# Optimization experiments

Measured on AMD Instinct MI355X. Metric: run time of the kernel, lower is better.

The kernel has to match this reference:

```python
import jax, jax.numpy as jnp
import numpy as np

B, C, H, W = 8, 384, 32, 32
NH = 6
HD = C // NH          # 64
T = H * W             # 1024
EPS = 1e-5            # torch InstanceNorm2d default


def setup_inputs() -> dict:
    key = jax.random.key(0)
    ks = jax.random.split(key, 8)
    s = 1.0 / np.sqrt(C)  # keep pre-softmax logits in a sane range
    x = jax.random.normal(ks[0], (B, C, H, W), dtype=jnp.float32)
    Wq = jax.random.normal(ks[1], (C, C), dtype=jnp.float32) * s
    Wk = jax.random.normal(ks[2], (C, C), dtype=jnp.float32) * s
    Wv = jax.random.normal(ks[3], (C, C), dtype=jnp.float32) * s
    head_w = jax.random.normal(ks[4], (NH, NH), dtype=jnp.float32) * (1.0 / np.sqrt(NH))
    gamma = jnp.ones((NH,), dtype=jnp.float32)
    beta = jnp.zeros((NH,), dtype=jnp.float32)
    projW = jax.random.normal(ks[5], (C, C), dtype=jnp.float32) * s
    projb = jnp.zeros((C,), dtype=jnp.float32)
    return {"x": x, "Wq": Wq, "Wk": Wk, "Wv": Wv, "head_w": head_w,
            "gamma": gamma, "beta": beta, "projW": projW, "projb": projb}


def reference(x, Wq, Wk, Wv, head_w, gamma, beta, projW, projb):
    b, c, h, w = x.shape
    t = h * w
    scale = HD ** (-0.5)
    xf = x.reshape(b, c, t)                               # [B,C,T]
    # 1x1 convs == channel GEMMs; conv weight [Cout,Cin]
    q = jnp.einsum('oc,bct->bot', Wq, xf).reshape(b, NH, HD, t)
    k = jnp.einsum('oc,bct->bot', Wk, xf).reshape(b, NH, HD, t)
    v = jnp.einsum('oc,bct->bot', Wv, xf).reshape(b, NH, HD, t)
    # raw scores [B,h,T,T], scaled
    scores = jnp.einsum('bhdq,bhdt->bhqt', q, k) * scale
    # cross-head 1x1 conv mix: out-head g from in-head h
    mixed = jnp.einsum('gh,bhqt->bgqt', head_w, scores)
    attn = jax.nn.softmax(mixed, axis=-1)
    # InstanceNorm2d over spatial dims (q,T) per (b,head), biased variance
    mean = jnp.mean(attn, axis=(2, 3), keepdims=True)
    var = jnp.var(attn, axis=(2, 3), keepdims=True)
    attn = (attn - mean) * jax.lax.rsqrt(var + EPS)
    attn = attn * gamma[None, :, None, None] + beta[None, :, None, None]
    # value matmul: v is [B,h,d,T]
    out = jnp.einsum('bhqt,bhdt->bhqd', attn, v)          # [B,h,T,d]
    # faithful row-major reshape (matches torch .view(B, T, C))
    out = out.reshape(b, t, c)
    y = out @ projW.T + projb                              # Linear(C,C)
    return jnp.transpose(y, (0, 2, 1)).reshape(b, c, h, w)
```

## Files before the change

kernel.cpp:

```cpp
#include <hip/hip_runtime.h>
#include <hip/hip_bf16.h>
#include <cstdint>

typedef __bf16 bf16_t;
typedef __bf16 bf16x8 __attribute__((ext_vector_type(8)));
typedef float  f32x4  __attribute__((ext_vector_type(4)));

#define MFMA16(a, b, c) __builtin_amdgcn_mfma_f32_16x16x32_bf16((a), (b), (c), 0, 0, 0)

constexpr int BB = 8, CC = 384, NHH = 6, TT = 1024;

union U8 { uint4 u; bf16_t h[8]; };
union U2 { unsigned int u; bf16_t h[2]; };

struct CastArgs {
    const void* src[9];
    bf16_t*     dst[9];
    int         n[9];
};

__global__ __launch_bounds__(256) void cast_kernel(CastArgs a)
{
    const bool isbf = (((const unsigned short*)a.src[5])[0] == 0x3F80u);
    const int ai = blockIdx.y;
    const int n  = a.n[ai];
    bf16_t* dst  = a.dst[ai];
    const int t0     = (blockIdx.x * 256 + threadIdx.x) * 8;
    const int stride = gridDim.x * 256 * 8;
    if (isbf) {
        const bf16_t* s = (const bf16_t*)a.src[ai];
        for (int idx = t0; idx < n; idx += stride) {
            if (idx + 8 <= n) *(uint4*)(dst + idx) = *(const uint4*)(s + idx);
            else for (int j = 0; idx + j < n; ++j) dst[idx + j] = s[idx + j];
        }
    } else {
        const float* s = (const float*)a.src[ai];
        for (int idx = t0; idx < n; idx += stride) {
            if (idx + 8 <= n) {
                f32x4 v0 = *(const f32x4*)(s + idx);
                f32x4 v1 = *(const f32x4*)(s + idx + 4);
                U8 o;
                #pragma unroll
                for (int j = 0; j < 4; ++j) { o.h[j] = (bf16_t)v0[j]; o.h[4 + j] = (bf16_t)v1[j]; }
                *(uint4*)(dst + idx) = o.u;
            } else for (int j = 0; idx + j < n; ++j) dst[idx + j] = (bf16_t)s[idx + j];
        }
    }
}

__global__ __launch_bounds__(256) void qkv_kernel(
    const bf16_t* __restrict__ x,
    const bf16_t* __restrict__ Wq,
    const bf16_t* __restrict__ Wk,
    const bf16_t* __restrict__ Wv,
    const bf16_t* __restrict__ head_w,
    bf16_t* __restrict__ Qmix,
    bf16_t* __restrict__ kT,
    bf16_t* __restrict__ vm)
{
    const int og = blockIdx.x;
    const int tt = blockIdx.y;
    const int b  = blockIdx.z;
    const int t0 = tt * 64;
    const int tid  = threadIdx.x;
    const int lane = tid & 63;
    const int wid  = tid >> 6;
    const int quad = lane >> 4;
    const int l16  = lane & 15;

    __shared__ __align__(16) bf16_t xT[64][CC + 8];
    __shared__ float smixL[36];

    if (tid < 36) smixL[tid] = 0.125f * (float)head_w[tid];
    {
        const bf16_t* xb = x + (size_t)b * CC * TT;
        const int tq = tid & 7;
        const int cp = tid >> 3;
        #pragma unroll
        for (int pass = 0; pass < 6; ++pass) {
            const int c = (pass * 32 + cp) * 2;
            U8 r0, r1;
            r0.u = *(const uint4*)(xb + (size_t)c * TT + t0 + tq * 8);
            r1.u = *(const uint4*)(xb + (size_t)(c + 1) * TT + t0 + tq * 8);
            #pragma unroll
            for (int j = 0; j < 8; ++j) {
                U2 p; p.h[0] = r0.h[j]; p.h[1] = r1.h[j];
                *(unsigned int*)&xT[tq * 8 + j][c] = p.u;
            }
        }
    }
    __syncthreads();

    const bf16_t* W = (og < 2) ? Wq : (og < 4) ? Wk : Wv;
    const int obase = (og & 1) * 192 + wid * 48;

    if (og < 4) {
        f32x4 acc[3][4];
        const f32x4 zero = {0.f, 0.f, 0.f, 0.f};
        #pragma unroll
        for (int mi = 0; mi < 3; ++mi)
            #pragma unroll
            for (int ni = 0; ni < 4; ++ni) acc[mi][ni] = zero;

        for (int k0 = 0; k0 < CC; k0 += 32) {
            bf16x8 afr[3];
            #pragma unroll
            for (int mi = 0; mi < 3; ++mi)
                afr[mi] = *(const bf16x8*)(W + (size_t)(obase + mi * 16 + l16) * CC + k0 + quad * 8);
            #pragma unroll
            for (int ni = 0; ni < 4; ++ni) {
                bf16x8 bfr = *(const bf16x8*)&xT[ni * 16 + l16][k0 + quad * 8];
                #pragma unroll
                for (int mi = 0; mi < 3; ++mi)
                    acc[mi][ni] = MFMA16(afr[mi], bfr, acc[mi][ni]);
            }
        }

        if (og < 2) {
            for (int g = 0; g < 6; ++g) {
                bf16_t* dst = Qmix + (size_t)(b * NHH + g) * TT * CC;
                #pragma unroll
                for (int mi = 0; mi < 3; ++mi)
                    #pragma unroll
                    for (int ni = 0; ni < 4; ++ni) {
                        const int o0 = obase + mi * 16 + quad * 4;
                        const int tl = t0 + ni * 16 + l16;
                        const float m = smixL[g * 6 + (o0 >> 6)];
                        U2 lo2, hi2;
                        lo2.h[0] = (bf16_t)(acc[mi][ni][0] * m); lo2.h[1] = (bf16_t)(acc[mi][ni][1] * m);
                        hi2.h[0] = (bf16_t)(acc[mi][ni][2] * m); hi2.h[1] = (bf16_t)(acc[mi][ni][3] * m);
                        uint2 pk; pk.x = lo2.u; pk.y = hi2.u;
                        *(uint2*)(dst + (size_t)tl * CC + o0) = pk;
                    }
            }
        } else {
            #pragma unroll
            for (int mi = 0; mi < 3; ++mi)
                #pragma unroll
                for (int ni = 0; ni < 4; ++ni) {
                    const int o0 = obase + mi * 16 + quad * 4;
                    const int tl = t0 + ni * 16 + l16;
                    U2 lo2, hi2;
                    lo2.h[0] = (bf16_t)acc[mi][ni][0]; lo2.h[1] = (bf16_t)acc[mi][ni][1];
                    hi2.h[0] = (bf16_t)acc[mi][ni][2]; hi2.h[1] = (bf16_t)acc[mi][ni][3];
                    uint2 pk; pk.x = lo2.u; pk.y = hi2.u;
                    *(uint2*)(kT + ((size_t)b * TT + tl) * CC + o0) = pk;
                }
        }
    } else {
        f32x4 acc[4][3];
        const f32x4 zero = {0.f, 0.f, 0.f, 0.f};
        #pragma unroll
        for (int mi = 0; mi < 4; ++mi)
            #pragma unroll
            for (int ni = 0; ni < 3; ++ni) acc[mi][ni] = zero;

        for (int k0 = 0; k0 < CC; k0 += 32) {
            bf16x8 bfr[3];
            #pragma unroll
            for (int ni = 0; ni < 3; ++ni)
                bfr[ni] = *(const bf16x8*)(W + (size_t)(obase + ni * 16 + l16) * CC + k0 + quad * 8);
            #pragma unroll
            for (int mi = 0; mi < 4; ++mi) {
                bf16x8 afr = *(const bf16x8*)&xT[mi * 16 + l16][k0 + quad * 8];
                #pragma unroll
                for (int ni = 0; ni < 3; ++ni)
                    acc[mi][ni] = MFMA16(afr, bfr[ni], acc[mi][ni]);
            }
        }

        #pragma unroll
        for (int mi = 0; mi < 4; ++mi)
            #pragma unroll
            for (int ni = 0; ni < 3; ++ni) {
                const int ol  = obase + ni * 16 + l16;
                const int tl0 = mi * 16 + quad * 4;
                U2 lo2, hi2;
                lo2.h[0] = (bf16_t)acc[mi][ni][0]; lo2.h[1] = (bf16_t)acc[mi][ni][1];
                hi2.h[0] = (bf16_t)acc[mi][ni][2]; hi2.h[1] = (bf16_t)acc[mi][ni][3];
                uint2 pk; pk.x = lo2.u; pk.y = hi2.u;
                *(uint2*)(vm + ((size_t)b * CC + ol) * TT + t0 + tl0) = pk;
            }
    }
}

__global__ __launch_bounds__(256) void vrow_kernel(const bf16_t* __restrict__ vm,
                                                   float* __restrict__ vrs)
{
    const int bg = blockIdx.x;
    const int d  = threadIdx.x & 63;
    const int qr = threadIdx.x >> 6;
    const bf16_t* row = vm + ((size_t)(bg / 6) * CC + (bg % 6) * 64 + d) * TT + qr * 256;
    float s = 0.f;
    for (int i = 0; i < 256; i += 8) {
        U8 v; v.u = *(const uint4*)(row + i);
        #pragma unroll
        for (int j = 0; j < 8; ++j) s += (float)v.h[j];
    }
    __shared__ float red[4][64];
    red[qr][d] = s;
    __syncthreads();
    if (qr == 0) vrs[bg * 64 + d] = red[0][d] + red[1][d] + red[2][d] + red[3][d];
}

__global__ __launch_bounds__(256, 3) void fused_attn(
    const bf16_t* __restrict__ Qmix,
    const bf16_t* __restrict__ kT,
    const bf16_t* __restrict__ vm,
    float* __restrict__ Uhat,
    float* __restrict__ sumsq)
{
    const int L  = blockIdx.x;
    const int b  = L & 7;
    const int rr = L >> 3;
    const int qt = rr & 15;
    const int g  = rr >> 4;
    const int qbase = qt * 64;
    const int tid = threadIdx.x, lane = tid & 63, wid = tid >> 6;
    const int quad = lane >> 4, l16 = lane & 15;
    const int Msub = (wid & 1) * 64;
    const int Nsub = (wid >> 1) * 32;

    __shared__ __align__(16) bf16_t sm[12288];
    bf16_t* At = sm;
    bf16_t* Bt = sm + 8192;
    bf16_t* Ps = sm;
    bf16_t* Vt = sm + 4096;
    __shared__ float lred[4][2][16], l2red[4][2][16];
    __shared__ float lrowS[64];

    const bf16_t* kTb = kT + (size_t)b * TT * CC;
    const bf16_t* Qb  = Qmix + ((size_t)(b * NHH + g) * TT + qbase) * CC;
    const bf16_t* Vb  = vm + ((size_t)b * CC + g * 64) * TT;

    float lacc[2] = {0.f, 0.f}, l2acc[2] = {0.f, 0.f};
    f32x4 U[4];
    const f32x4 zero = {0.f, 0.f, 0.f, 0.f};
    #pragma unroll
    for (int n2 = 0; n2 < 4; ++n2) U[n2] = zero;

    for (int tt = 0; tt < 8; ++tt) {
        f32x4 S[4][2];
        #pragma unroll
        for (int mi = 0; mi < 4; ++mi)
            #pragma unroll
            for (int ni = 0; ni < 2; ++ni) S[mi][ni] = zero;

        for (int kk = 0; kk < 6; ++kk) {
            __syncthreads();
            #pragma unroll
            for (int it = 0; it < 4; ++it) {
                const int id = it * 256 + tid;
                const int row = id >> 3, ch = id & 7;
                U8 v; v.u = *(const uint4*)(kTb + (size_t)(tt * 128 + row) * CC + kk * 64 + ch * 8);
                *(uint4*)&At[row * 64 + ((ch ^ (row & 7)) * 8)] = v.u;
            }
            #pragma unroll
            for (int it = 0; it < 2; ++it) {
                const int id = it * 256 + tid;
                const int row = id >> 3, ch = id & 7;
                U8 v; v.u = *(const uint4*)(Qb + (size_t)row * CC + kk * 64 + ch * 8);
                *(uint4*)&Bt[row * 64 + ((ch ^ (row & 7)) * 8)] = v.u;
            }
            __syncthreads();
            #pragma unroll
            for (int k2 = 0; k2 < 2; ++k2) {
                const int sw = ((k2 * 4 + quad) ^ (l16 & 7)) * 8;
                bf16x8 a[4], bq[2];
                #pragma unroll
                for (int mi = 0; mi < 4; ++mi)
                    a[mi] = *(const bf16x8*)&At[(Msub + mi * 16 + l16) * 64 + sw];
                #pragma unroll
                for (int ni = 0; ni < 2; ++ni)
                    bq[ni] = *(const bf16x8*)&Bt[(Nsub + ni * 16 + l16) * 64 + sw];
                #pragma unroll
                for (int mi = 0; mi < 4; ++mi)
                    #pragma unroll
                    for (int ni = 0; ni < 2; ++ni)
                        S[mi][ni] = MFMA16(a[mi], bq[ni], S[mi][ni]);
            }
        }

        #pragma unroll
        for (int mi = 0; mi < 4; ++mi)
            #pragma unroll
            for (int ni = 0; ni < 2; ++ni)
                #pragma unroll
                for (int r = 0; r < 4; ++r) {
                    const float p = __expf(fminf(S[mi][ni][r], 60.0f));
                    S[mi][ni][r] = p;
                    lacc[ni]  += p;
                    l2acc[ni] += p * p;
                }

        __syncthreads();

        #pragma unroll
        for (int it = 0; it < 4; ++it) {
            const int id = it * 256 + tid;
            const int row = id >> 4, ch = id & 15;
            U8 v; v.u = *(const uint4*)(Vb + (size_t)row * TT + tt * 128 + ch * 8);
            *(uint4*)&Vt[row * 128 + ((((ch & 7) ^ (row & 7)) | (ch & 8)) * 8)] = v.u;
        }

        #pragma unroll
        for (int h = 0; h < 2; ++h) {
            if ((wid & 1) == h) {
                #pragma unroll
                for (int mi = 0; mi < 4; ++mi) {
                    const int tc = mi * 2 + (quad >> 1);
                    #pragma unroll
                    for (int ni = 0; ni < 2; ++ni) {
                        const int q = Nsub + ni * 16 + l16;
                        U2 lo2, hi2;
                        lo2.h[0] = (bf16_t)S[mi][ni][0]; lo2.h[1] = (bf16_t)S[mi][ni][1];
                        hi2.h[0] = (bf16_t)S[mi][ni][2]; hi2.h[1] = (bf16_t)S[mi][ni][3];
                        uint2 pk; pk.x = lo2.u; pk.y = hi2.u;
                        *(uint2*)&Ps[q * 64 + ((tc ^ (l16 & 7)) * 8) + (quad & 1) * 4] = pk;
                    }
                }
            }
            __syncthreads();
            bf16x8 ap[2];
            #pragma unroll
            for (int k2 = 0; k2 < 2; ++k2) {
                const int qa = wid * 16 + l16;
                ap[k2] = *(const bf16x8*)&Ps[qa * 64 + (((k2 * 4 + quad) ^ (l16 & 7)) * 8)];
            }
            #pragma unroll
            for (int n2 = 0; n2 < 4; ++n2) {
                const int d = n2 * 16 + l16;
                #pragma unroll
                for (int k2 = 0; k2 < 2; ++k2) {
                    const int tc = h * 8 + k2 * 4 + quad;
                    bf16x8 bv = *(const bf16x8*)&Vt[d * 128 + ((((tc & 7) ^ (l16 & 7)) | (tc & 8)) * 8)];
                    U[n2] = MFMA16(ap[k2], bv, U[n2]);
                }
            }
            __syncthreads();
        }
    }

    #pragma unroll
    for (int ni = 0; ni < 2; ++ni) {
        float l = lacc[ni], l2 = l2acc[ni];
        l  += __shfl_xor(l, 16, 64);  l  += __shfl_xor(l, 32, 64);
        l2 += __shfl_xor(l2, 16, 64); l2 += __shfl_xor(l2, 32, 64);
        if (quad == 0) { lred[wid][ni][l16] = l; l2red[wid][ni][l16] = l2; }
    }
    __syncthreads();
    if (tid < 64) {
        const int q = tid;
        const int w0 = (q >> 5) * 2, ni = (q >> 4) & 1, lo = q & 15;
        const float l  = lred[w0][ni][lo]  + lred[w0 + 1][ni][lo];
        const float l2 = l2red[w0][ni][lo] + l2red[w0 + 1][ni][lo];
        lrowS[q] = l;
        float c = l2 / (l * l);
        #pragma unroll
        for (int off = 1; off < 64; off <<= 1) c += __shfl_xor(c, off, 64);
        if (tid == 0) atomicAdd(&sumsq[b * NHH + g], c);
    }
    __syncthreads();

    float* Ub = Uhat + ((size_t)(b * NHH + g) * TT + qbase) * 64;
    #pragma unroll
    for (int r = 0; r < 4; ++r) {
        const int ql = wid * 16 + quad * 4 + r;
        const float invl = 1.0f / lrowS[ql];
        #pragma unroll
        for (int n2 = 0; n2 < 4; ++n2)
            Ub[(size_t)ql * 64 + n2 * 16 + l16] = U[n2][r] * invl;
    }
}

__global__ __launch_bounds__(256) void proj_kernel(
    const float* __restrict__ Uhat,
    const float* __restrict__ vrs,
    const float* __restrict__ sumsq,
    const bf16_t* __restrict__ gamma,
    const bf16_t* __restrict__ beta,
    const bf16_t* __restrict__ projW,
    const bf16_t* __restrict__ projb,
    float* __restrict__ out)
{
    const int ts = blockIdx.x;
    const int b  = blockIdx.y;
    const int t0 = ts * 32;
    const int tid = threadIdx.x, lane = tid & 63, wid = tid >> 6;
    const int quad = lane >> 4, l16 = lane & 15;

    __shared__ float Ac[6], Cc[6], pb[CC];
    if (tid < 6) {
        const float ss  = sumsq[b * NHH + tid];
        const float var = fmaxf(ss - 1.0f, 0.0f) * (1.0f / 1048576.0f);
        const float a   = (float)gamma[tid] * rsqrtf(var + 1e-5f);
        Ac[tid] = a;
        Cc[tid] = (float)beta[tid] - a * (1.0f / 1024.0f);
    }
    for (int i = tid; i < CC; i += 256) pb[i] = (float)projb[i];
    __syncthreads();

    f32x4 acc[6][2];
    const f32x4 zero = {0.f, 0.f, 0.f, 0.f};
    #pragma unroll
    for (int mi = 0; mi < 6; ++mi)
        #pragma unroll
        for (int ni = 0; ni < 2; ++ni) acc[mi][ni] = zero;

    const float* Ub = Uhat + (size_t)b * TT * CC;
    for (int k0 = 0; k0 < CC; k0 += 32) {
        bf16x8 bfr[2];
        #pragma unroll
        for (int ni = 0; ni < 2; ++ni) {
            const int tl = t0 + ni * 16 + l16;
            const int baseoff = tl * CC + k0 + quad * 8;
            f32x4 u0 = *(const f32x4*)(Ub + baseoff);
            f32x4 u1 = *(const f32x4*)(Ub + baseoff + 4);
            U8 z;
            #pragma unroll
            for (int j = 0; j < 8; ++j) {
                const int off = baseoff + j;
                const int h = off >> 16;
                const int d = off & 63;
                const float uv = (j < 4) ? u0[j] : u1[j - 4];
                z.h[j] = (bf16_t)(Ac[h] * uv + Cc[h] * vrs[(b * NHH + h) * 64 + d]);
            }
            bfr[ni] = *(const bf16x8*)&z;
        }
        #pragma unroll
        for (int mi = 0; mi < 6; ++mi) {
            const int o = wid * 96 + mi * 16 + l16;
            bf16x8 afr = *(const bf16x8*)(projW + (size_t)o * CC + k0 + quad * 8);
            #pragma unroll
            for (int ni = 0; ni < 2; ++ni)
                acc[mi][ni] = MFMA16(afr, bfr[ni], acc[mi][ni]);
        }
    }

    #pragma unroll
    for (int mi = 0; mi < 6; ++mi)
        #pragma unroll
        for (int ni = 0; ni < 2; ++ni)
            #pragma unroll
            for (int r = 0; r < 4; ++r) {
                const int o  = wid * 96 + mi * 16 + quad * 4 + r;
                const int tl = t0 + ni * 16 + l16;
                out[((size_t)b * CC + o) * TT + tl] = acc[mi][ni][r] + pb[o];
            }
}

extern "C" void kernel_launch(void* const* d_in, const int* in_sizes, int n_in,
                              void* d_out, int out_size, void* d_ws, size_t ws_size,
                              hipStream_t stream)
{
    float* outp = (float*)d_out;
    char* ws = (char*)d_ws;

    size_t off = 0;
    auto alloc = [&](size_t bytes) {
        void* p = ws + off;
        off += (bytes + 255) & ~(size_t)255;
        return p;
    };

    const size_t szQ = (size_t)BB * TT * CC * sizeof(bf16_t);

    bf16_t* cx  = (bf16_t*)alloc(szQ);
    bf16_t* cWq = (bf16_t*)alloc((size_t)CC * CC * 2);
    bf16_t* cWk = (bf16_t*)alloc((size_t)CC * CC * 2);
    bf16_t* cWv = (bf16_t*)alloc((size_t)CC * CC * 2);
    bf16_t* cPW = (bf16_t*)alloc((size_t)CC * CC * 2);
    bf16_t* chw = (bf16_t*)alloc(64 * 2);
    bf16_t* cg  = (bf16_t*)alloc(64 * 2);
    bf16_t* cb  = (bf16_t*)alloc(64 * 2);
    bf16_t* cpb = (bf16_t*)alloc(CC * 2);
    bf16_t* Qm  = (bf16_t*)alloc((size_t)BB * NHH * TT * CC * 2);
    bf16_t* kT  = (bf16_t*)alloc(szQ);
    bf16_t* vm  = (bf16_t*)alloc(szQ);
    float*  Uh  = (float*)alloc((size_t)BB * NHH * TT * 64 * 4);
    float*  vr  = (float*)alloc(48 * 64 * 4);
    float*  sq  = (float*)alloc(48 * 4);

    CastArgs ca;
    bf16_t* dsts[9] = {cx, cWq, cWk, cWv, chw, cg, cb, cPW, cpb};
    for (int i = 0; i < 9; ++i) {
        ca.src[i] = d_in[i];
        ca.dst[i] = dsts[i];
        ca.n[i]   = in_sizes[i];
    }

    hipMemsetAsync(sq, 0, 48 * sizeof(float), stream);
    cast_kernel<<<dim3(192, 9), 256, 0, stream>>>(ca);
    qkv_kernel<<<dim3(6, 16, 8), 256, 0, stream>>>(cx, cWq, cWk, cWv, chw, Qm, kT, vm);
    vrow_kernel<<<48, 256, 0, stream>>>(vm, vr);
    fused_attn<<<768, 256, 0, stream>>>(Qm, kT, vm, Uh, sq);
    proj_kernel<<<dim3(32, 8), 256, 0, stream>>>(Uh, vr, sq, cg, cb, cPW, cpb, outp);
}
```

Baseline: 217.7 us.

## Apply head mix in attention kernel, prefetch tiles, fuse V row sums

The head-mixed Q tensor (six copies per batch) is no longer materialized in the QKV kernel. A single unmixed Q is written, and the attention kernel scales it by the head-mix weights while staging it into shared memory. The attention kernel also prefetches the next K/Q tiles and V tiles into registers so global loads overlap compute. The P·V stage now uses a single 128-wide P tile, which drops two barriers per iteration but enlarges shared memory. The separate vrow kernel is folded into the QKV epilogue through atomics, and the memset now covers vrs plus sumsq, which relies on them being allocated next to each other.

```diff
diff --git a/kernel.cpp b/kernel.cpp
--- a/kernel.cpp
+++ b/kernel.cpp
@@ -53,10 +53,10 @@
     const bf16_t* __restrict__ Wq,
     const bf16_t* __restrict__ Wk,
     const bf16_t* __restrict__ Wv,
-    const bf16_t* __restrict__ head_w,
-    bf16_t* __restrict__ Qmix,
+    bf16_t* __restrict__ qT,
     bf16_t* __restrict__ kT,
-    bf16_t* __restrict__ vm)
+    bf16_t* __restrict__ vm,
+    float* __restrict__ vrs)
 {
     const int og = blockIdx.x;
     const int tt = blockIdx.y;
@@ -69,9 +69,7 @@
     const int l16  = lane & 15;
 
     __shared__ __align__(16) bf16_t xT[64][CC + 8];
-    __shared__ float smixL[36];
-
-    if (tid < 36) smixL[tid] = 0.125f * (float)head_w[tid];
+
     {
         const bf16_t* xb = x + (size_t)b * CC * TT;
         const int tq = tid & 7;
@@ -116,37 +114,19 @@
             }
         }
 
-        if (og < 2) {
-            for (int g = 0; g < 6; ++g) {
-                bf16_t* dst = Qmix + (size_t)(b * NHH + g) * TT * CC;
-                #pragma unroll
-                for (int mi = 0; mi < 3; ++mi)
-                    #pragma unroll
-                    for (int ni = 0; ni < 4; ++ni) {
-                        const int o0 = obase + mi * 16 + quad * 4;
-                        const int tl = t0 + ni * 16 + l16;
-                        const float m = smixL[g * 6 + (o0 >> 6)];
-                        U2 lo2, hi2;
-                        lo2.h[0] = (bf16_t)(acc[mi][ni][0] * m); lo2.h[1] = (bf16_t)(acc[mi][ni][1] * m);
-                        hi2.h[0] = (bf16_t)(acc[mi][ni][2] * m); hi2.h[1] = (bf16_t)(acc[mi][ni][3] * m);
-                        uint2 pk; pk.x = lo2.u; pk.y = hi2.u;
-                        *(uint2*)(dst + (size_t)tl * CC + o0) = pk;
-                    }
-            }
-        } else {
-            #pragma unroll
-            for (int mi = 0; mi < 3; ++mi)
-                #pragma unroll
-                for (int ni = 0; ni < 4; ++ni) {
-                    const int o0 = obase + mi * 16 + quad * 4;
-                    const int tl = t0 + ni * 16 + l16;
-                    U2 lo2, hi2;
-                    lo2.h[0] = (bf16_t)acc[mi][ni][0]; lo2.h[1] = (bf16_t)acc[mi][ni][1];
-                    hi2.h[0] = (bf16_t)acc[mi][ni][2]; hi2.h[1] = (bf16_t)acc[mi][ni][3];
-                    uint2 pk; pk.x = lo2.u; pk.y = hi2.u;
-                    *(uint2*)(kT + ((size_t)b * TT + tl) * CC + o0) = pk;
-                }
-        }
+        bf16_t* dst = (og < 2) ? qT : kT;
+        #pragma unroll
+        for (int mi = 0; mi < 3; ++mi)
+            #pragma unroll
+            for (int ni = 0; ni < 4; ++ni) {
+                const int o0 = obase + mi * 16 + quad * 4;
+                const int tl = t0 + ni * 16 + l16;
+                U2 lo2, hi2;
+                lo2.h[0] = (bf16_t)acc[mi][ni][0]; lo2.h[1] = (bf16_t)acc[mi][ni][1];
+                hi2.h[0] = (bf16_t)acc[mi][ni][2]; hi2.h[1] = (bf16_t)acc[mi][ni][3];
+                uint2 pk; pk.x = lo2.u; pk.y = hi2.u;
+                *(uint2*)(dst + ((size_t)b * TT + tl) * CC + o0) = pk;
+            }
     } else {
         f32x4 acc[4][3];
         const f32x4 zero = {0.f, 0.f, 0.f, 0.f};
@@ -170,43 +150,31 @@
         }
 
         #pragma unroll
-        for (int mi = 0; mi < 4; ++mi)
-            #pragma unroll
-            for (int ni = 0; ni < 3; ++ni) {
-                const int ol  = obase + ni * 16 + l16;
+        for (int ni = 0; ni < 3; ++ni) {
+            const int ol = obase + ni * 16 + l16;
+            float s = 0.f;
+            #pragma unroll
+            for (int mi = 0; mi < 4; ++mi) {
                 const int tl0 = mi * 16 + quad * 4;
                 U2 lo2, hi2;
                 lo2.h[0] = (bf16_t)acc[mi][ni][0]; lo2.h[1] = (bf16_t)acc[mi][ni][1];
                 hi2.h[0] = (bf16_t)acc[mi][ni][2]; hi2.h[1] = (bf16_t)acc[mi][ni][3];
                 uint2 pk; pk.x = lo2.u; pk.y = hi2.u;
                 *(uint2*)(vm + ((size_t)b * CC + ol) * TT + t0 + tl0) = pk;
-            }
+                s += acc[mi][ni][0] + acc[mi][ni][1] + acc[mi][ni][2] + acc[mi][ni][3];
+            }
+            s += __shfl_xor(s, 16, 64);
+            s += __shfl_xor(s, 32, 64);
+            if (quad == 0) atomicAdd(&vrs[b * CC + ol], s);
+        }
     }
 }
 
-__global__ __launch_bounds__(256) void vrow_kernel(const bf16_t* __restrict__ vm,
-                                                   float* __restrict__ vrs)
-{
-    const int bg = blockIdx.x;
-    const int d  = threadIdx.x & 63;
-    const int qr = threadIdx.x >> 6;
-    const bf16_t* row = vm + ((size_t)(bg / 6) * CC + (bg % 6) * 64 + d) * TT + qr * 256;
-    float s = 0.f;
-    for (int i = 0; i < 256; i += 8) {
-        U8 v; v.u = *(const uint4*)(row + i);
-        #pragma unroll
-        for (int j = 0; j < 8; ++j) s += (float)v.h[j];
-    }
-    __shared__ float red[4][64];
-    red[qr][d] = s;
-    __syncthreads();
-    if (qr == 0) vrs[bg * 64 + d] = red[0][d] + red[1][d] + red[2][d] + red[3][d];
-}
-
 __global__ __launch_bounds__(256, 3) void fused_attn(
-    const bf16_t* __restrict__ Qmix,
+    const bf16_t* __restrict__ qT,
     const bf16_t* __restrict__ kT,
     const bf16_t* __restrict__ vm,
+    const bf16_t* __restrict__ head_w,
     float* __restrict__ Uhat,
     float* __restrict__ sumsq)
 {
@@ -221,17 +189,25 @@
     const int Msub = (wid & 1) * 64;
     const int Nsub = (wid >> 1) * 32;
 
-    __shared__ __align__(16) bf16_t sm[12288];
+    __shared__ __align__(16) bf16_t sm[16384];
     bf16_t* At = sm;
     bf16_t* Bt = sm + 8192;
     bf16_t* Ps = sm;
-    bf16_t* Vt = sm + 4096;
+    bf16_t* Vt = sm + 8192;
     __shared__ float lred[4][2][16], l2red[4][2][16];
     __shared__ float lrowS[64];
 
+    float smix6[6];
+    #pragma unroll
+    for (int h = 0; h < 6; ++h) smix6[h] = 0.125f * (float)head_w[g * 6 + h];
+
     const bf16_t* kTb = kT + (size_t)b * TT * CC;
-    const bf16_t* Qb  = Qmix + ((size_t)(b * NHH + g) * TT + qbase) * CC;
+    const bf16_t* Qb  = qT + ((size_t)b * TT + qbase) * CC;
     const bf16_t* Vb  = vm + ((size_t)b * CC + g * 64) * TT;
+
+    const int arow = tid >> 1, ach0 = (tid & 1) * 4;
+    const int brow = tid >> 2, bch  = tid & 3;
+    const int vrow = tid >> 2, vch0 = (tid & 3) * 4;
 
     float lacc[2] = {0.f, 0.f}, l2acc[2] = {0.f, 0.f};
     f32x4 U[4];
@@ -239,7 +215,32 @@
     #pragma unroll
     for (int n2 = 0; n2 < 4; ++n2) U[n2] = zero;
 
+    uint4 pA[4], pB[2], pV[4];
+    auto loadAB = [&](int ttp, int kkp) {
+        #pragma unroll
+        for (int it = 0; it < 4; ++it) {
+            const int id = it * 256 + tid;
+            const int row = id >> 3, ch = id & 7;
+            pA[it] = *(const uint4*)(kTb + (size_t)(ttp * 128 + row) * CC + kkp * 64 + ch * 8);
+        }
+        #pragma unroll
+        for (int it = 0; it < 2; ++it) {
+            const int id = it * 256 + tid;
+            const int row = id >> 3, ch = id & 7;
+            pB[it] = *(const uint4*)(Qb + (size_t)row * CC + kkp * 64 + ch * 8);
+        }
+    };
+
+    loadAB(0, 0);
+
     for (int tt = 0; tt < 8; ++tt) {
+        #pragma unroll
+        for (int it = 0; it < 4; ++it) {
+            const int id = it * 256 + tid;
+            const int row = id >> 4, ch = id & 15;
+            pV[it] = *(const uint4*)(Vb + (size_t)row * TT + tt * 128 + ch * 8);
+        }
+
         f32x4 S[4][2];
         #pragma unroll
         for (int mi = 0; mi < 4; ++mi)
@@ -252,15 +253,23 @@
             for (int it = 0; it < 4; ++it) {
                 const int id = it * 256 + tid;
                 const int row = id >> 3, ch = id & 7;
-                U8 v; v.u = *(const uint4*)(kTb + (size_t)(tt * 128 + row) * CC + kk * 64 + ch * 8);
-                *(uint4*)&At[row * 64 + ((ch ^ (row & 7)) * 8)] = v.u;
-            }
+                *(uint4*)&At[row * 64 + ((ch ^ (row & 7)) * 8)] = pA[it];
+            }
+            const float m = smix6[kk];
             #pragma unroll
             for (int it = 0; it < 2; ++it) {
                 const int id = it * 256 + tid;
                 const int row = id >> 3, ch = id & 7;
-                U8 v; v.u = *(const uint4*)(Qb + (size_t)row * CC + kk * 64 + ch * 8);
-                *(uint4*)&Bt[row * 64 + ((ch ^ (row & 7)) * 8)] = v.u;
+                U8 v; v.u = pB[it];
+                U8 o;
+                #pragma unroll
+                for (int j = 0; j < 8; ++j) o.h[j] = (bf16_t)((float)v.h[j] * m);
+                *(uint4*)&Bt[row * 64 + ((ch ^ (row & 7)) * 8)] = o.u;
+            }
+            {
+                int nkk = kk + 1, ntt = tt;
+                if (nkk == 6) { nkk = 0; ntt = tt + 1; }
+                if (ntt < 8) loadAB(ntt, nkk);
             }
             __syncthreads();
             #pragma unroll
@@ -299,45 +308,35 @@
         for (int it = 0; it < 4; ++it) {
             const int id = it * 256 + tid;
             const int row = id >> 4, ch = id & 15;
-            U8 v; v.u = *(const uint4*)(Vb + (size_t)row * TT + tt * 128 + ch * 8);
-            *(uint4*)&Vt[row * 128 + ((((ch & 7) ^ (row & 7)) | (ch & 8)) * 8)] = v.u;
-        }
-
-        #pragma unroll
-        for (int h = 0; h < 2; ++h) {
-            if ((wid & 1) == h) {
-                #pragma unroll
-                for (int mi = 0; mi < 4; ++mi) {
-                    const int tc = mi * 2 + (quad >> 1);
-                    #pragma unroll
-                    for (int ni = 0; ni < 2; ++ni) {
-                        const int q = Nsub + ni * 16 + l16;
-                        U2 lo2, hi2;
-                        lo2.h[0] = (bf16_t)S[mi][ni][0]; lo2.h[1] = (bf16_t)S[mi][ni][1];
-                        hi2.h[0] = (bf16_t)S[mi][ni][2]; hi2.h[1] = (bf16_t)S[mi][ni][3];
-                        uint2 pk; pk.x = lo2.u; pk.y = hi2.u;
-                        *(uint2*)&Ps[q * 64 + ((tc ^ (l16 & 7)) * 8) + (quad & 1) * 4] = pk;
-                    }
-                }
-            }
-            __syncthreads();
-            bf16x8 ap[2];
-            #pragma unroll
-            for (int k2 = 0; k2 < 2; ++k2) {
-                const int qa = wid * 16 + l16;
-                ap[k2] = *(const bf16x8*)&Ps[qa * 64 + (((k2 * 4 + quad) ^ (l16 & 7)) * 8)];
-            }
+            *(uint4*)&Vt[row * 128 + ((((ch & 7) ^ (row & 7)) | (ch & 8)) * 8)] = pV[it];
+        }
+        #pragma unroll
+        for (int mi = 0; mi < 4; ++mi) {
+            const int tc = (Msub >> 3) + mi * 2 + (quad >> 1);
+            const int off = (quad & 1) * 4;
+            #pragma unroll
+            for (int ni = 0; ni < 2; ++ni) {
+                const int q = Nsub + ni * 16 + l16;
+                U2 lo2, hi2;
+                lo2.h[0] = (bf16_t)S[mi][ni][0]; lo2.h[1] = (bf16_t)S[mi][ni][1];
+                hi2.h[0] = (bf16_t)S[mi][ni][2]; hi2.h[1] = (bf16_t)S[mi][ni][3];
+                uint2 pk; pk.x = lo2.u; pk.y = hi2.u;
+                *(uint2*)&Ps[q * 128 + ((((tc & 7) ^ (q & 7)) | (tc & 8)) * 8) + off] = pk;
+            }
+        }
+        __syncthreads();
+
+        const int qa = wid * 16 + l16;
+        #pragma unroll
+        for (int k2 = 0; k2 < 4; ++k2) {
+            const int tc = k2 * 4 + quad;
+            bf16x8 ap = *(const bf16x8*)&Ps[qa * 128 + ((((tc & 7) ^ (qa & 7)) | (tc & 8)) * 8)];
             #pragma unroll
             for (int n2 = 0; n2 < 4; ++n2) {
                 const int d = n2 * 16 + l16;
-                #pragma unroll
-                for (int k2 = 0; k2 < 2; ++k2) {
-                    const int tc = h * 8 + k2 * 4 + quad;
-                    bf16x8 bv = *(const bf16x8*)&Vt[d * 128 + ((((tc & 7) ^ (l16 & 7)) | (tc & 8)) * 8)];
-                    U[n2] = MFMA16(ap[k2], bv, U[n2]);
-                }
-            }
-            __syncthreads();
+                bf16x8 bv = *(const bf16x8*)&Vt[d * 128 + ((((tc & 7) ^ (d & 7)) | (tc & 8)) * 8)];
+                U[n2] = MFMA16(ap, bv, U[n2]);
+            }
         }
     }
 
@@ -423,7 +422,7 @@
                 const int h = off >> 16;
                 const int d = off & 63;
                 const float uv = (j < 4) ? u0[j] : u1[j - 4];
-                z.h[j] = (bf16_t)(Ac[h] * uv + Cc[h] * vrs[(b * NHH + h) * 64 + d]);
+                z.h[j] = (bf16_t)(Ac[h] * uv + Cc[h] * vrs[b * CC + h * 64 + d]);
             }
             bfr[ni] = *(const bf16x8*)&z;
         }
@@ -474,11 +473,11 @@
     bf16_t* cg  = (bf16_t*)alloc(64 * 2);
     bf16_t* cb  = (bf16_t*)alloc(64 * 2);
     bf16_t* cpb = (bf16_t*)alloc(CC * 2);
-    bf16_t* Qm  = (bf16_t*)alloc((size_t)BB * NHH * TT * CC * 2);
+    bf16_t* qT  = (bf16_t*)alloc(szQ);
     bf16_t* kT  = (bf16_t*)alloc(szQ);
     bf16_t* vm  = (bf16_t*)alloc(szQ);
     float*  Uh  = (float*)alloc((size_t)BB * NHH * TT * 64 * 4);
-    float*  vr  = (float*)alloc(48 * 64 * 4);
+    float*  vr  = (float*)alloc(BB * CC * 4);
     float*  sq  = (float*)alloc(48 * 4);
 
     CastArgs ca;
@@ -489,10 +488,9 @@
         ca.n[i]   = in_sizes[i];
     }
 
-    hipMemsetAsync(sq, 0, 48 * sizeof(float), stream);
+    hipMemsetAsync(vr, 0, BB * CC * 4 + 256, stream);
     cast_kernel<<<dim3(192, 9), 256, 0, stream>>>(ca);
-    qkv_kernel<<<dim3(6, 16, 8), 256, 0, stream>>>(cx, cWq, cWk, cWv, chw, Qm, kT, vm);
-    vrow_kernel<<<48, 256, 0, stream>>>(vm, vr);
-    fused_attn<<<768, 256, 0, stream>>>(Qm, kT, vm, Uh, sq);
+    qkv_kernel<<<dim3(6, 16, 8), 256, 0, stream>>>(cx, cWq, cWk, cWv, qT, kT, vm, vr);
+    fused_attn<<<768, 256, 0, stream>>>(qT, kT, vm, chw, Uh, sq);
     proj_kernel<<<dim3(32, 8), 256, 0, stream>>>(Uh, vr, sq, cg, cb, cPW, cpb, outp);
 }
```

Measured after the change: 358.1 us. +64.5%, slower.
